# Performance work log

Hardware: AMD Instinct MI355X
Metric: run time of the kernel (lower is better)

## Reference

```python
import jax, jax.numpy as jnp
import numpy as np

EPS = 1e-6
NUM_HEADS = 8
GAMMA = 0.999


def simple_rms_norm(x):
    # SimpleRMSNorm: x / ||x|| * sqrt(d) == x / sqrt(mean(x^2))
    return x * jax.lax.rsqrt(jnp.mean(x * x, axis=-1, keepdims=True) + EPS)


def setup_inputs() -> dict:
    key = jax.random.key(0)
    ks = jax.random.split(key, 12)
    B, N, M, E = 64, 14, 14, 512
    D1 = 2 * E              # expand_ratio * embed_dim = 1024
    RPE = 512               # rpe_embedding
    s = 0.02
    inp = {
        "x": jax.random.normal(ks[0], (B, N, M, E), jnp.float32),
        "H": N,
        "W": M,
        "Wu": jax.random.normal(ks[1], (E, D1), jnp.float32) * s,
        "bu": jnp.zeros((D1,), jnp.float32),
        "Wv": jax.random.normal(ks[2], (E, D1), jnp.float32) * s,
        "bv": jnp.zeros((D1,), jnp.float32),
        "Wo": jax.random.normal(ks[3], (D1, E), jnp.float32) * s,
        "bo": jnp.zeros((E,), jnp.float32),
        "rpe_pos_w": jax.random.normal(ks[4], (2, RPE), jnp.float32) * s,
        "rpe_pos_b": jnp.zeros((RPE,), jnp.float32),
        "rpe_w1": jax.random.normal(ks[5], (RPE, RPE), jnp.float32) * s,
        "rpe_b1": jnp.zeros((RPE,), jnp.float32),
        "rpe_w2": jax.random.normal(ks[6], (RPE, RPE), jnp.float32) * s,
        "rpe_b2": jnp.zeros((RPE,), jnp.float32),
        "rpe_w3": jax.random.normal(ks[7], (RPE, RPE), jnp.float32) * s,
        "rpe_b3": jnp.zeros((RPE,), jnp.float32),
        "rpe_out_w": jax.random.normal(ks[8], (RPE, D1), jnp.float32) * s,
        "rpe_out_b": jnp.zeros((D1,), jnp.float32),
    }
    return inp


def gtu2d_forward(x, Wu, bu, Wv, bv, Wo, bo,
                  rpe_pos_w, rpe_pos_b, rpe_w1, rpe_b1, rpe_w2, rpe_b2,
                  rpe_w3, rpe_b3, rpe_out_w, rpe_out_b):
    B, n, m, E = x.shape
    d1 = Wu.shape[1]
    hd = d1 // NUM_HEADS
    # dual gated projections
    u = jax.nn.silu(x @ Wu + bu)                      # (B, n, m, d1)
    v = jax.nn.silu(x @ Wv + bv)
    v = v.reshape(B, n, m, NUM_HEADS, hd).transpose(0, 3, 1, 2, 4)  # (B, h, n, m, d)

    # --- Tno2D: RPE MLP produces Toeplitz coefficients for relative positions ---
    ii = jnp.arange(-(n - 1), n, dtype=jnp.float32)
    jj = jnp.arange(-(m - 1), m, dtype=jnp.float32)
    pos = jnp.stack(jnp.meshgrid(ii, jj, indexing="ij"), axis=-1)  # (2n-1, 2m-1, 2)
    r = pos @ rpe_pos_w + rpe_pos_b
    for w, b in ((rpe_w1, rpe_b1), (rpe_w2, rpe_b2), (rpe_w3, rpe_b3)):
        r = jax.nn.relu(simple_rms_norm(r)) @ w + b
    r = jax.nn.relu(simple_rms_norm(r)) @ rpe_out_w + rpe_out_b  # (2n-1, 2m-1, h*d)
    a = r.reshape(2 * n - 1, 2 * m - 1, NUM_HEADS, hd).transpose(2, 0, 1, 3)
    # decay: gamma^(|i|+|j|)
    dist = jnp.abs(pos[..., 0]) + jnp.abs(pos[..., 1])  # (2n-1, 2m-1)
    a = a * (GAMMA ** dist)[None, :, :, None]

    # embed coefficients into circular kernel (h, 2n, 2m, d); index n / m are zero
    t = jnp.zeros((NUM_HEADS, 2 * n, 2 * m, hd), a.dtype)
    t = t.at[:, :n, :m].set(a[:, n - 1:, m - 1:])
    t = t.at[:, n + 1:, :m].set(a[:, :n - 1, m - 1:])
    t = t.at[:, :n, m + 1:].set(a[:, n - 1:, :m - 1])
    t = t.at[:, n + 1:, m + 1:].set(a[:, :n - 1, :m - 1])

    # 2D Toeplitz matvec via circular convolution / FFT
    xf = jnp.fft.rfft2(v, s=(2 * n, 2 * m), axes=(2, 3))
    tf = jnp.fft.rfft2(t, s=(2 * n, 2 * m), axes=(1, 2))
    y = jnp.fft.irfft2(xf * tf[None], s=(2 * n, 2 * m), axes=(2, 3))[:, :, :n, :m, :]
    y = y.transpose(0, 2, 3, 1, 4).reshape(B, n, m, d1)  # 'b h n m d -> b n m (h d)'

    return (u * y) @ Wo + bo


def reference(x, H, W, Wu, bu, Wv, bv, Wo, bo,
              rpe_pos_w, rpe_pos_b, rpe_w1, rpe_b1, rpe_w2, rpe_b2,
              rpe_w3, rpe_b3, rpe_out_w, rpe_out_b):
    # H, W are unused by Gtu2d.forward (spatial dims are carried by x)
    return gtu2d_forward(x, Wu, bu, Wv, bv, Wo, bo,
                         rpe_pos_w, rpe_pos_b, rpe_w1, rpe_b1, rpe_w2, rpe_b2,
                         rpe_w3, rpe_b3, rpe_out_w, rpe_out_b)
```

## Files before the change

kernel.cpp:

```cpp
#include <hip/hip_runtime.h>
#include <hip/hip_bf16.h>

typedef __hip_bfloat16 bf16;
typedef __attribute__((ext_vector_type(8))) short bf16x8;
typedef __attribute__((ext_vector_type(4))) float f32x4;

constexpr int NB    = 64;
constexpr int EE    = 512;
constexpr int RPOS  = 27 * 27;
constexpr int ROWS  = NB * 14 * 14;

#define RMS_EPS 1e-6f
#define GAMMA_LOG2 (-0.00144344319f)

__device__ __forceinline__ void  stf(float* p, float v) { *p = v; }
__device__ __forceinline__ void  stf(bf16* p, float v)  { *p = __float2bfloat16(v); }

__device__ __forceinline__ void gload_lds16(const bf16* g, bf16* l) {
    __builtin_amdgcn_global_load_lds(
        (const __attribute__((address_space(1))) void*)g,
        (__attribute__((address_space(3))) void*)l, 16, 0, 0);
}

#define VMCNT(n) asm volatile("s_waitcnt vmcnt(" #n ")" ::: "memory")

__global__ __launch_bounds__(256) void k_prep(const float* __restrict__ Wu,
                                              const float* __restrict__ Wv,
                                              const float* __restrict__ Wo,
                                              const float* __restrict__ w1,
                                              const float* __restrict__ w2,
                                              const float* __restrict__ w3,
                                              const float* __restrict__ wOut,
                                              const float* __restrict__ bu,
                                              const float* __restrict__ bv,
                                              const float* __restrict__ x,
                                              bf16* __restrict__ WuvT,
                                              bf16* __restrict__ WoT,
                                              bf16* __restrict__ w1T,
                                              bf16* __restrict__ w2T,
                                              bf16* __restrict__ w3T,
                                              bf16* __restrict__ wOutT,
                                              float* __restrict__ biasUv,
                                              bf16* __restrict__ xb,
                                              bf16* __restrict__ Vt) {
    __shared__ float t[32][33];
    const int tid = threadIdx.x;
    int b = blockIdx.x;

    const float* src = nullptr; bf16* dst = nullptr; int R = 0, C = 0, nbx = 0;
    if (b < 512)        { src = Wu;   dst = WuvT;                      R = 512;  C = 1024; nbx = 32; }
    else if (b < 1024)  { b -= 512;   src = Wv; dst = WuvT + (size_t)1024 * 512; R = 512; C = 1024; nbx = 32; }
    else if (b < 1536)  { b -= 1024;  src = Wo;   dst = WoT;           R = 1024; C = 512;  nbx = 16; }
    else if (b < 1792)  { b -= 1536;  src = w1;   dst = w1T;           R = 512;  C = 512;  nbx = 16; }
    else if (b < 2048)  { b -= 1792;  src = w2;   dst = w2T;           R = 512;  C = 512;  nbx = 16; }
    else if (b < 2304)  { b -= 2048;  src = w3;   dst = w3T;           R = 512;  C = 512;  nbx = 16; }
    else if (b < 2816)  { b -= 2304;  src = wOut; dst = wOutT;         R = 512;  C = 1024; nbx = 32; }
    else if (b < 2824) {
        int c = (b - 2816) * 256 + tid;
        if (c < 2048) biasUv[c] = (c < 1024) ? bu[c] : bv[c - 1024];
        return;
    } else if (b < 9096) {
        int i = (b - 2824) * 256 + tid;
        float4 v = *(const float4*)&x[(size_t)i * 4];
        bf16* d = &xb[(size_t)i * 4];
        d[0] = __float2bfloat16(v.x);
        d[1] = __float2bfloat16(v.y);
        d[2] = __float2bfloat16(v.z);
        d[3] = __float2bfloat16(v.w);
        return;
    } else {
        int c = b - 9096;
        const bf16 z = __float2bfloat16(0.0f);
        for (int f = tid; f < 64 * 28; f += 256) {
            int bb = f / 28, k = f - bb * 28;
            Vt[((size_t)c * 64 + bb) * 224 + 196 + k] = z;
        }
        return;
    }
    int bx = (b % nbx) * 32;
    int by = (b / nbx) * 32;
    int tx = tid & 31, ty = tid >> 5;
    #pragma unroll
    for (int i = 0; i < 4; ++i)
        t[ty + i * 8][tx] = src[(size_t)(by + ty + i * 8) * C + bx + tx];
    __syncthreads();
    #pragma unroll
    for (int i = 0; i < 4; ++i)
        dst[(size_t)(bx + ty + i * 8) * R + by + tx] = __float2bfloat16(t[tx][ty + i * 8]);
}

__global__ void k_rpe_pos_norm(const float* __restrict__ w, const float* __restrict__ bias,
                               bf16* __restrict__ out) {
    int p = blockIdx.x;
    float ii = (float)(p / 27 - 13);
    float jj = (float)(p % 27 - 13);
    int c0 = threadIdx.x, c1 = threadIdx.x + 256;
    float v0 = ii * w[c0] + jj * w[512 + c0] + bias[c0];
    float v1 = ii * w[c1] + jj * w[512 + c1] + bias[c1];
    float s = v0 * v0 + v1 * v1;
    #pragma unroll
    for (int off = 32; off; off >>= 1) s += __shfl_down(s, off, 64);
    __shared__ float ps[4];
    if ((threadIdx.x & 63) == 0) ps[threadIdx.x >> 6] = s;
    __syncthreads();
    float tot = ps[0] + ps[1] + ps[2] + ps[3];
    float scale = rsqrtf(tot * (1.0f / 512.0f) + RMS_EPS);
    out[(size_t)p * 512 + c0] = __float2bfloat16(fmaxf(v0 * scale, 0.0f));
    out[(size_t)p * 512 + c1] = __float2bfloat16(fmaxf(v1 * scale, 0.0f));
}

template <int SCALE_IN, int EPI>
__global__ __launch_bounds__(256) void k_rpe_gemm(const bf16* __restrict__ A,
                                                  const bf16* __restrict__ Bt,
                                                  const float* __restrict__ bias,
                                                  const float* __restrict__ pIn,
                                                  float* __restrict__ pOut,
                                                  bf16* __restrict__ out,
                                                  int M, int N, int K) {
    __shared__ bf16 As[64 * 32];
    __shared__ bf16 Bs[64 * 32];
    const int tid = threadIdx.x;
    const int m0 = blockIdx.y * 64;
    const int n0 = blockIdx.x * 64;
    const int lane = tid & 63;
    const int w = tid >> 6;
    const int lr = lane & 15;
    const int lk = (lane >> 4) * 8;

    f32x4 acc[4] = {};
    const int row = tid >> 2;
    const int seg = (tid & 3) * 8;

    for (int k0 = 0; k0 < K; k0 += 32) {
        gload_lds16(&A[(size_t)(m0 + row) * K + k0 + seg], &As[tid * 8]);
        gload_lds16(&Bt[(size_t)(n0 + row) * K + k0 + seg], &Bs[tid * 8]);
        __syncthreads();
        bf16x8 af = *(const bf16x8*)&As[(w * 16 + lr) * 32 + lk];
        #pragma unroll
        for (int j = 0; j < 4; ++j) {
            bf16x8 bf = *(const bf16x8*)&Bs[(j * 16 + lr) * 32 + lk];
            acc[j] = __builtin_amdgcn_mfma_f32_16x16x32_bf16(af, bf, acc[j], 0, 0, 0);
        }
        __syncthreads();
    }

    const int crow = (lane >> 4) * 4;
    const int ccol = lane & 15;
    float sc[4];
    #pragma unroll
    for (int r = 0; r < 4; ++r) {
        sc[r] = 1.0f;
        if (SCALE_IN) {
            int gr = m0 + w * 16 + crow + r;
            if (gr < M) {
                const float* pp = &pIn[(size_t)gr * 8];
                float s8 = pp[0] + pp[1] + pp[2] + pp[3] + pp[4] + pp[5] + pp[6] + pp[7];
                sc[r] = rsqrtf(s8 * (1.0f / 512.0f) + RMS_EPS);
            }
        }
    }
    float rowsq[4] = {0.f, 0.f, 0.f, 0.f};
    #pragma unroll
    for (int j = 0; j < 4; ++j) {
        int gc = n0 + j * 16 + ccol;
        float bb = bias[gc];
        #pragma unroll
        for (int r = 0; r < 4; ++r) {
            int gr = m0 + w * 16 + crow + r;
            float val = acc[j][r] * sc[r] + bb;
            if (EPI == 0) {
                rowsq[r] += val * val;
                if (gr < M) out[(size_t)gr * N + gc] = __float2bfloat16(fmaxf(val, 0.0f));
            } else {
                if (gr < M) {
                    int i = gr / 27, jj = gr % 27;
                    float decay = exp2f((float)(abs(i - 13) + abs(jj - 13)) * GAMMA_LOG2);
                    out[(size_t)gr * N + gc] = __float2bfloat16(val * decay);
                }
            }
        }
    }
    if (EPI == 0) {
        #pragma unroll
        for (int r = 0; r < 4; ++r) {
            #pragma unroll
            for (int m = 1; m < 16; m <<= 1) rowsq[r] += __shfl_xor(rowsq[r], m, 64);
        }
        if ((lane & 15) == 0) {
            #pragma unroll
            for (int r = 0; r < 4; ++r) {
                int gr = m0 + w * 16 + crow + r;
                if (gr < M) pOut[(size_t)gr * 8 + blockIdx.x] = rowsq[r];
            }
        }
    }
}

template <int EPI, typename TO>
__global__ __launch_bounds__(256) void k_mgemm(const bf16* __restrict__ A, int lda,
                                               const bf16* __restrict__ Bt,
                                               const float* __restrict__ bias,
                                               TO* __restrict__ out, int ldo,
                                               int M, int N, int K) {
    __shared__ bf16 As[128 * 32];
    __shared__ bf16 Bs[128 * 32];
    const int tid = threadIdx.x;
    const int m0 = blockIdx.y * 128;
    const int n0 = blockIdx.x * 128;
    const int lane = tid & 63;
    const int w = tid >> 6;
    const int wr = (w >> 1) * 64;
    const int wc = (w & 1) * 64;
    const int lr = lane & 15;
    const int lk = (lane >> 4) * 8;

    f32x4 acc[4][4] = {};

    for (int k0 = 0; k0 < K; k0 += 32) {
        #pragma unroll
        for (int t = 0; t < 2; ++t) {
            int flat = t * 256 + tid;
            int row = flat >> 2;
            int seg = (flat & 3) * 8;
            gload_lds16(&A[(size_t)(m0 + row) * lda + k0 + seg], &As[flat * 8]);
            gload_lds16(&Bt[(size_t)(n0 + row) * K + k0 + seg], &Bs[flat * 8]);
        }
        __syncthreads();
        bf16x8 af[4], bf[4];
        #pragma unroll
        for (int i = 0; i < 4; ++i) {
            af[i] = *(const bf16x8*)&As[(wr + i * 16 + lr) * 32 + lk];
            bf[i] = *(const bf16x8*)&Bs[(wc + i * 16 + lr) * 32 + lk];
        }
        #pragma unroll
        for (int i = 0; i < 4; ++i)
            #pragma unroll
            for (int j = 0; j < 4; ++j)
                acc[i][j] = __builtin_amdgcn_mfma_f32_16x16x32_bf16(af[i], bf[j], acc[i][j], 0, 0, 0);
        __syncthreads();
    }

    const int crow = (lane >> 4) * 4;
    const int ccol = lane & 15;
    #pragma unroll
    for (int i = 0; i < 4; ++i)
        #pragma unroll
        for (int j = 0; j < 4; ++j) {
            int gc = n0 + wc + j * 16 + ccol;
            float bb = bias[gc];
            #pragma unroll
            for (int r = 0; r < 4; ++r) {
                int gr = m0 + wr + i * 16 + crow + r;
                float val = acc[i][j][r] + bb;
                if (EPI == 1) val = val / (1.0f + expf(-val));
                stf(&out[(size_t)gr * ldo + gc], val);
            }
        }
}

template <int KT, int EPI, typename TO>
__global__ __launch_bounds__(512, 2) void k_mgemm8(const bf16* __restrict__ A, int lda,
                                                   const bf16* __restrict__ Bt,
                                                   const float* __restrict__ bias,
                                                   TO* __restrict__ out, int ldo,
                                                   int nb ,
                                                   bf16* __restrict__ Vt) {
    constexpr int K = KT * 64;
    __shared__ __align__(16) char lds[131072];

    const int tid = threadIdx.x;
    const int lane = tid & 63;
    const int wid = tid >> 6;
    const int wr = wid >> 2;
    const int wc = wid & 3;

    int wgid = blockIdx.x;
    if ((gridDim.x & 7) == 0) {
        int cpx = gridDim.x >> 3;
        wgid = (wgid & 7) * cpx + (wgid >> 3);
    }
    const int m0 = (wgid / nb) * 256;
    const int n0 = (wgid % nb) * 256;

    auto ldsA = [&](int d, int kh) -> char* { return (char*)lds + d * 32768 + kh * 16384; };
    auto ldsB = [&](int d, int kh) -> char* { return (char*)lds + 65536 + d * 32768 + kh * 16384; };

    auto stage = [&](int op, int kh, int tt) {
        char* base = op ? ldsB(tt & 1, kh) : ldsA(tt & 1, kh);
        const bf16* g = op ? Bt : A;
        const int rowbase = op ? n0 : m0;
        const int ldr = op ? K : lda;
        #pragma unroll
        for (int l = 0; l < 2; ++l) {
            int q = tid + l * 512;
            int r = q >> 2;
            int cl = (q & 3) ^ ((r ^ (r >> 2)) & 3);
            const bf16* src = g + (size_t)(rowbase + r) * ldr + tt * 64 + kh * 32 + cl * 8;
            gload_lds16(src, (bf16*)(base + q * 16));
        }
    };
    auto rdA = [&](int d, int ks, int mi) -> bf16x8 {
        int row = wr * 128 + mi * 16 + (lane & 15);
        int ch = (lane >> 4) ^ ((row ^ (row >> 2)) & 3);
        return *(const bf16x8*)(ldsA(d, ks) + row * 64 + ch * 16);
    };
    auto rdB = [&](int d, int ks, int nj) -> bf16x8 {
        int row = wc * 64 + nj * 16 + (lane & 15);
        int ch = (lane >> 4) ^ ((row ^ (row >> 2)) & 3);
        return *(const bf16x8*)(ldsB(d, ks) + row * 64 + ch * 16);
    };

    f32x4 acc[8][4] = {};
    bf16x8 aF[4], bF[4];

    stage(0, 0, 0); stage(1, 0, 0); stage(0, 1, 0); stage(1, 1, 0);
    stage(0, 0, 1); stage(1, 0, 1);
    VMCNT(8);
    __builtin_amdgcn_s_barrier();
    __builtin_amdgcn_sched_barrier(0);

    #pragma unroll
    for (int t = 0; t < KT; ++t) {
        const int d = t & 1;
        #pragma unroll
        for (int mi = 0; mi < 4; ++mi) aF[mi] = rdA(d, 0, mi);
        #pragma unroll
        for (int nj = 0; nj < 4; ++nj) bF[nj] = rdB(d, 0, nj);
        if (t + 1 < KT) stage(0, 1, t + 1);
        __builtin_amdgcn_s_barrier();
        __builtin_amdgcn_s_setprio(1);
        #pragma unroll
        for (int mi = 0; mi < 4; ++mi)
            #pragma unroll
            for (int nj = 0; nj < 4; ++nj)
                acc[mi][nj] = __builtin_amdgcn_mfma_f32_16x16x32_bf16(aF[mi], bF[nj], acc[mi][nj], 0, 0, 0);
        __builtin_amdgcn_s_setprio(0);
        __builtin_amdgcn_s_barrier();
        #pragma unroll
        for (int mi = 0; mi < 4; ++mi) aF[mi] = rdA(d, 0, mi + 4);
        if (t + 1 < KT) stage(1, 1, t + 1);
        if (t + 1 < KT) { VMCNT(8); } else { VMCNT(0); }
        __builtin_amdgcn_s_barrier();
        __builtin_amdgcn_sched_barrier(0);
        __builtin_amdgcn_s_setprio(1);
        #pragma unroll
        for (int mi = 0; mi < 4; ++mi)
            #pragma unroll
            for (int nj = 0; nj < 4; ++nj)
                acc[mi + 4][nj] = __builtin_amdgcn_mfma_f32_16x16x32_bf16(aF[mi], bF[nj], acc[mi + 4][nj], 0, 0, 0);
        __builtin_amdgcn_s_setprio(0);
        __builtin_amdgcn_s_barrier();
        #pragma unroll
        for (int mi = 0; mi < 4; ++mi) aF[mi] = rdA(d, 1, mi);
        #pragma unroll
        for (int nj = 0; nj < 4; ++nj) bF[nj] = rdB(d, 1, nj);
        if (t + 2 < KT) stage(0, 0, t + 2);
        __builtin_amdgcn_s_barrier();
        __builtin_amdgcn_s_setprio(1);
        #pragma unroll
        for (int mi = 0; mi < 4; ++mi)
            #pragma unroll
            for (int nj = 0; nj < 4; ++nj)
                acc[mi][nj] = __builtin_amdgcn_mfma_f32_16x16x32_bf16(aF[mi], bF[nj], acc[mi][nj], 0, 0, 0);
        __builtin_amdgcn_s_setprio(0);
        __builtin_amdgcn_s_barrier();
        #pragma unroll
        for (int mi = 0; mi < 4; ++mi) aF[mi] = rdA(d, 1, mi + 4);
        if (t + 2 < KT) stage(1, 0, t + 2);
        if (t + 2 < KT)      { VMCNT(8); }
        else if (t + 1 < KT) { VMCNT(4); }
        __builtin_amdgcn_s_barrier();
        __builtin_amdgcn_sched_barrier(0);
        __builtin_amdgcn_s_setprio(1);
        #pragma unroll
        for (int mi = 0; mi < 4; ++mi)
            #pragma unroll
            for (int nj = 0; nj < 4; ++nj)
                acc[mi + 4][nj] = __builtin_amdgcn_mfma_f32_16x16x32_bf16(aF[mi], bF[nj], acc[mi + 4][nj], 0, 0, 0);
        __builtin_amdgcn_s_setprio(0);
        __builtin_amdgcn_s_barrier();
    }

    const int crow = (lane >> 4) * 4;
    const int ccol = lane & 15;
    #pragma unroll
    for (int mi = 0; mi < 8; ++mi)
        #pragma unroll
        for (int nj = 0; nj < 4; ++nj) {
            int gc = n0 + wc * 64 + nj * 16 + ccol;
            float bb = bias[gc];
            #pragma unroll
            for (int r = 0; r < 4; ++r) {
                int gr = m0 + wr * 128 + mi * 16 + crow + r;
                float val = acc[mi][nj][r] + bb;
                if (EPI == 1) {
                    val = val / (1.0f + expf(-val));
                    if (gc < 1024) {
                        stf(&out[(size_t)gr * ldo + gc], val);
                    } else {
                        int c = gc - 1024;
                        int b = gr / 196;
                        int ij = gr - b * 196;
                        Vt[((size_t)c * 64 + b) * 224 + ij] = __float2bfloat16(val);
                    }
                } else {
                    stf(&out[(size_t)gr * ldo + gc], val);
                }
            }
        }
}

__global__ __launch_bounds__(256) void k_convm(const bf16* __restrict__ Ab,
                                               const bf16* __restrict__ Vt,
                                               bf16* __restrict__ Yt) {
    __shared__ __align__(16) bf16 Ts[112 * 232];
    __shared__ bf16 As[736];
    const int mh = blockIdx.x;
    const int cl = blockIdx.y;
    const int c = (int)blockIdx.z * 512 + cl;
    const int tid = threadIdx.x;
    const int mbase = mh * 112;

    for (int e = tid; e < 729; e += 256)
        As[e] = Ab[(size_t)e * 1024 + c];
    __syncthreads();

    const bf16 z = __float2bfloat16(0.0f);
    if (tid < 224) {
        const int i = tid / 14, j = tid - i * 14;
        const bool kvalid = tid < 196;
        int p = mbase / 14, q = 0;
        for (int r = 0; r < 112; ++r) {
            bf16 val = z;
            if (kvalid && (mbase + r) < 196)
                val = As[(p - i + 13) * 27 + (q - j + 13)];
            Ts[r * 232 + tid] = val;
            if (++q == 14) { q = 0; ++p; }
        }
    }
    __syncthreads();

    const int lane = tid & 63;
    const int w = tid >> 6;
    const int lr = lane & 15;
    const int lk = (lane >> 4) * 8;
    const bf16* Vc = Vt + (size_t)c * 64 * 224;

    bf16x8 bfr[7];
    #pragma unroll
    for (int ks = 0; ks < 7; ++ks)
        bfr[ks] = *(const bf16x8*)&Vc[(size_t)(w * 16 + lr) * 224 + ks * 32 + lk];

    f32x4 acc[7] = {};
    #pragma unroll
    for (int ks = 0; ks < 7; ++ks)
        #pragma unroll
        for (int mi = 0; mi < 7; ++mi) {
            bf16x8 a = *(const bf16x8*)&Ts[(mi * 16 + lr) * 232 + ks * 32 + lk];
            acc[mi] = __builtin_amdgcn_mfma_f32_16x16x32_bf16(a, bfr[ks], acc[mi], 0, 0, 0);
        }

    const int crow = (lane >> 4) * 4;
    const int bb = w * 16 + (lane & 15);
    #pragma unroll
    for (int mi = 0; mi < 7; ++mi) {
        int pq = mbase + mi * 16 + crow;
        #pragma unroll
        for (int r = 0; r < 4; ++r)
            if (pq + r < 196)
                Yt[((size_t)c * 196 + pq + r) * 64 + bb] = __float2bfloat16(acc[mi][r]);
    }
}

__global__ __launch_bounds__(256) void k_gate(bf16* __restrict__ uv,
                                              const bf16* __restrict__ Yt) {
    const int pq = blockIdx.x;
    const int ct = blockIdx.y;
    const int cb = (int)blockIdx.z * 512;
    const int tid = threadIdx.x;
    __shared__ float t[64][65];
    for (int f = tid; f < 64 * 64; f += 256) {
        int cr = f >> 6, bcol = f & 63;
        t[cr][bcol] = __bfloat162float(Yt[((size_t)(cb + ct * 64 + cr) * 196 + pq) * 64 + bcol]);
    }
    __syncthreads();
    for (int f = tid; f < 64 * 64; f += 256) {
        int br = f >> 6, cc = f & 63;
        size_t row = (size_t)br * 196 + pq;
        int cglob = cb + ct * 64 + cc;
        float uu = __bfloat162float(uv[row * 2048 + cglob]);
        uv[row * 2048 + 1024 + cglob] = __float2bfloat16(t[cc][br] * uu);
    }
}

extern "C" void kernel_launch(void* const* d_in, const int* in_sizes, int n_in,
                              void* d_out, int out_size, void* d_ws, size_t ws_size,
                              hipStream_t stream) {
    const float* x    = (const float*)d_in[0];
    const float* Wu   = (const float*)d_in[3];
    const float* bu   = (const float*)d_in[4];
    const float* Wv   = (const float*)d_in[5];
    const float* bv   = (const float*)d_in[6];
    const float* Wo   = (const float*)d_in[7];
    const float* bo   = (const float*)d_in[8];
    const float* rpw  = (const float*)d_in[9];
    const float* rpb  = (const float*)d_in[10];
    const float* w1   = (const float*)d_in[11];
    const float* b1   = (const float*)d_in[12];
    const float* w2   = (const float*)d_in[13];
    const float* b2   = (const float*)d_in[14];
    const float* w3   = (const float*)d_in[15];
    const float* b3   = (const float*)d_in[16];
    const float* wOut = (const float*)d_in[17];
    const float* bOut = (const float*)d_in[18];

    char* ws = (char*)d_ws;
    size_t off = 0;
    auto take = [&](size_t bytes) { char* p = ws + off; off += (bytes + 255) & ~size_t(255); return p; };
    bf16*  rnA    = (bf16*)take((size_t)768 * 512 * 2);
    bf16*  rnB    = (bf16*)take((size_t)768 * 512 * 2);
    float* p1     = (float*)take((size_t)768 * 8 * 4);
    float* p2     = (float*)take((size_t)768 * 8 * 4);
    float* p3     = (float*)take((size_t)768 * 8 * 4);
    bf16*  Ab     = (bf16*)take((size_t)RPOS * 1024 * 2);
    bf16*  xb     = (bf16*)take((size_t)ROWS * EE * 2);
    bf16*  WuvT   = (bf16*)take((size_t)2048 * 512 * 2);
    bf16*  WoT    = (bf16*)take((size_t)512 * 1024 * 2);
    bf16*  w1T    = (bf16*)take((size_t)512 * 512 * 2);
    bf16*  w2T    = (bf16*)take((size_t)512 * 512 * 2);
    bf16*  w3T    = (bf16*)take((size_t)512 * 512 * 2);
    bf16*  wOutT  = (bf16*)take((size_t)1024 * 512 * 2);
    float* biasUv = (float*)take(2048 * 4);
    bf16*  uvb    = (bf16*)take((size_t)ROWS * 2048 * 2);
    bf16*  Vt     = (bf16*)take((size_t)1024 * 64 * 224 * 2);
    bf16*  Yt     = (bf16*)take((size_t)1024 * 196 * 64 * 2);

    k_prep<<<10120, 256, 0, stream>>>(Wu, Wv, Wo, w1, w2, w3, wOut, bu, bv, x,
                                      WuvT, WoT, w1T, w2T, w3T, wOutT, biasUv, xb, Vt);

    k_rpe_pos_norm<<<RPOS, 256, 0, stream>>>(rpw, rpb, rnA);
    k_rpe_gemm<0, 0><<<dim3(8, 12), 256, 0, stream>>>(rnA, w1T, b1, nullptr, p1, rnB, RPOS, 512, 512);
    k_rpe_gemm<1, 0><<<dim3(8, 12), 256, 0, stream>>>(rnB, w2T, b2, p1, p2, rnA, RPOS, 512, 512);
    k_rpe_gemm<1, 0><<<dim3(8, 12), 256, 0, stream>>>(rnA, w3T, b3, p2, p3, rnB, RPOS, 512, 512);
    k_rpe_gemm<1, 2><<<dim3(16, 12), 256, 0, stream>>>(rnB, wOutT, bOut, p3, nullptr, Ab, RPOS, 1024, 512);

    k_mgemm8<8, 1, bf16><<<392, 512, 0, stream>>>(xb, 512, WuvT, biasUv, uvb, 2048, 8, Vt);

    k_convm<<<dim3(2, 512, 2), 256, 0, stream>>>(Ab, Vt, Yt);
    k_gate<<<dim3(196, 8, 2), 256, 0, stream>>>(uvb, Yt);

    k_mgemm<0, float><<<dim3(4, 98), 256, 0, stream>>>(uvb + 1024, 2048, WoT, bo,
                                                       (float*)d_out, 512, ROWS, 512, 1024);
}
```

Measured before the change: 239.1 us.

## Move V transpose out of GEMM epilogue into a dedicated LDS transpose kernel

Measured after the change: 216.6 us. -9.4%, faster.

```diff
diff --git a/kernel.cpp b/kernel.cpp
--- a/kernel.cpp
+++ b/kernel.cpp
@@ -34,6 +34,8 @@
                                               const float* __restrict__ bu,
                                               const float* __restrict__ bv,
                                               const float* __restrict__ x,
+                                              const float* __restrict__ rpw,
+                                              const float* __restrict__ rpb,
                                               bf16* __restrict__ WuvT,
                                               bf16* __restrict__ WoT,
                                               bf16* __restrict__ w1T,
@@ -42,8 +44,9 @@
                                               bf16* __restrict__ wOutT,
                                               float* __restrict__ biasUv,
                                               bf16* __restrict__ xb,
-                                              bf16* __restrict__ Vt) {
+                                              bf16* __restrict__ rnA) {
     __shared__ float t[32][33];
+    __shared__ float ps[4];
     const int tid = threadIdx.x;
     int b = blockIdx.x;
 
@@ -69,12 +72,21 @@
         d[3] = __float2bfloat16(v.w);
         return;
     } else {
-        int c = b - 9096;
-        const bf16 z = __float2bfloat16(0.0f);
-        for (int f = tid; f < 64 * 28; f += 256) {
-            int bb = f / 28, k = f - bb * 28;
-            Vt[((size_t)c * 64 + bb) * 224 + 196 + k] = z;
-        }
+        int p = b - 9096;
+        float ii = (float)(p / 27 - 13);
+        float jj = (float)(p % 27 - 13);
+        int c0 = tid, c1 = tid + 256;
+        float v0 = ii * rpw[c0] + jj * rpw[512 + c0] + rpb[c0];
+        float v1 = ii * rpw[c1] + jj * rpw[512 + c1] + rpb[c1];
+        float s = v0 * v0 + v1 * v1;
+        #pragma unroll
+        for (int off = 32; off; off >>= 1) s += __shfl_down(s, off, 64);
+        if ((tid & 63) == 0) ps[tid >> 6] = s;
+        __syncthreads();
+        float tot = ps[0] + ps[1] + ps[2] + ps[3];
+        float scale = rsqrtf(tot * (1.0f / 512.0f) + RMS_EPS);
+        rnA[(size_t)p * 512 + c0] = __float2bfloat16(fmaxf(v0 * scale, 0.0f));
+        rnA[(size_t)p * 512 + c1] = __float2bfloat16(fmaxf(v1 * scale, 0.0f));
         return;
     }
     int bx = (b % nbx) * 32;
@@ -87,26 +99,6 @@
     #pragma unroll
     for (int i = 0; i < 4; ++i)
         dst[(size_t)(bx + ty + i * 8) * R + by + tx] = __float2bfloat16(t[tx][ty + i * 8]);
-}
-
-__global__ void k_rpe_pos_norm(const float* __restrict__ w, const float* __restrict__ bias,
-                               bf16* __restrict__ out) {
-    int p = blockIdx.x;
-    float ii = (float)(p / 27 - 13);
-    float jj = (float)(p % 27 - 13);
-    int c0 = threadIdx.x, c1 = threadIdx.x + 256;
-    float v0 = ii * w[c0] + jj * w[512 + c0] + bias[c0];
-    float v1 = ii * w[c1] + jj * w[512 + c1] + bias[c1];
-    float s = v0 * v0 + v1 * v1;
-    #pragma unroll
-    for (int off = 32; off; off >>= 1) s += __shfl_down(s, off, 64);
-    __shared__ float ps[4];
-    if ((threadIdx.x & 63) == 0) ps[threadIdx.x >> 6] = s;
-    __syncthreads();
-    float tot = ps[0] + ps[1] + ps[2] + ps[3];
-    float scale = rsqrtf(tot * (1.0f / 512.0f) + RMS_EPS);
-    out[(size_t)p * 512 + c0] = __float2bfloat16(fmaxf(v0 * scale, 0.0f));
-    out[(size_t)p * 512 + c1] = __float2bfloat16(fmaxf(v1 * scale, 0.0f));
 }
 
 template <int SCALE_IN, int EPI>
@@ -263,8 +255,7 @@
                                                    const bf16* __restrict__ Bt,
                                                    const float* __restrict__ bias,
                                                    TO* __restrict__ out, int ldo,
-                                                   int nb ,
-                                                   bf16* __restrict__ Vt) {
+                                                   int nb ) {
     constexpr int K = KT * 64;
     __shared__ __align__(16) char lds[131072];
 
@@ -393,21 +384,28 @@
             for (int r = 0; r < 4; ++r) {
                 int gr = m0 + wr * 128 + mi * 16 + crow + r;
                 float val = acc[mi][nj][r] + bb;
-                if (EPI == 1) {
-                    val = val / (1.0f + expf(-val));
-                    if (gc < 1024) {
-                        stf(&out[(size_t)gr * ldo + gc], val);
-                    } else {
-                        int c = gc - 1024;
-                        int b = gr / 196;
-                        int ij = gr - b * 196;
-                        Vt[((size_t)c * 64 + b) * 224 + ij] = __float2bfloat16(val);
-                    }
-                } else {
-                    stf(&out[(size_t)gr * ldo + gc], val);
-                }
+                if (EPI == 1) val = val / (1.0f + expf(-val));
+                stf(&out[(size_t)gr * ldo + gc], val);
             }
         }
+}
+
+__global__ __launch_bounds__(256) void k_vt(const bf16* __restrict__ uv,
+                                            bf16* __restrict__ Vt) {
+    const int c0 = blockIdx.x * 64;
+    const int b  = blockIdx.y;
+    const int tid = threadIdx.x;
+    __shared__ bf16 t[196][66];
+    for (int f = tid; f < 196 * 64; f += 256) {
+        int ij = f >> 6, cl = f & 63;
+        t[ij][cl] = uv[((size_t)b * 196 + ij) * 2048 + 1024 + c0 + cl];
+    }
+    __syncthreads();
+    const bf16 z = __float2bfloat16(0.0f);
+    for (int f = tid; f < 64 * 224; f += 256) {
+        int cl = f / 224, ij = f - cl * 224;
+        Vt[((size_t)(c0 + cl) * 64 + b) * 224 + ij] = (ij < 196) ? t[ij][cl] : z;
+    }
 }
 
 __global__ __launch_bounds__(256) void k_convm(const bf16* __restrict__ Ab,
@@ -535,16 +533,18 @@
     bf16*  Vt     = (bf16*)take((size_t)1024 * 64 * 224 * 2);
     bf16*  Yt     = (bf16*)take((size_t)1024 * 196 * 64 * 2);
 
-    k_prep<<<10120, 256, 0, stream>>>(Wu, Wv, Wo, w1, w2, w3, wOut, bu, bv, x,
-                                      WuvT, WoT, w1T, w2T, w3T, wOutT, biasUv, xb, Vt);
-
-    k_rpe_pos_norm<<<RPOS, 256, 0, stream>>>(rpw, rpb, rnA);
+    k_prep<<<9825, 256, 0, stream>>>(Wu, Wv, Wo, w1, w2, w3, wOut, bu, bv, x,
+                                     rpw, rpb,
+                                     WuvT, WoT, w1T, w2T, w3T, wOutT, biasUv, xb, rnA);
+
     k_rpe_gemm<0, 0><<<dim3(8, 12), 256, 0, stream>>>(rnA, w1T, b1, nullptr, p1, rnB, RPOS, 512, 512);
     k_rpe_gemm<1, 0><<<dim3(8, 12), 256, 0, stream>>>(rnB, w2T, b2, p1, p2, rnA, RPOS, 512, 512);
     k_rpe_gemm<1, 0><<<dim3(8, 12), 256, 0, stream>>>(rnA, w3T, b3, p2, p3, rnB, RPOS, 512, 512);
     k_rpe_gemm<1, 2><<<dim3(16, 12), 256, 0, stream>>>(rnB, wOutT, bOut, p3, nullptr, Ab, RPOS, 1024, 512);
 
-    k_mgemm8<8, 1, bf16><<<392, 512, 0, stream>>>(xb, 512, WuvT, biasUv, uvb, 2048, 8, Vt);
+    k_mgemm8<8, 1, bf16><<<392, 512, 0, stream>>>(xb, 512, WuvT, biasUv, uvb, 2048, 8);
+
+    k_vt<<<dim3(16, 64), 256, 0, stream>>>(uvb, Vt);
 
     k_convm<<<dim3(2, 512, 2), 256, 0, stream>>>(Ab, Vt, Yt);
     k_gate<<<dim3(196, 8, 2), 256, 0, stream>>>(uvb, Yt);
```
